# Kernel tuning notes

Measured on AMD Instinct MI355X. Metric: run time of the kernel, lower is better.

Reference implementation:

```python
import jax, jax.numpy as jnp
import numpy as np

B, S = 16, 4096
E_ENC, E_DEC, H = 1024, 1024, 512


def setup_inputs() -> dict:
    key = jax.random.key(0)
    ks = jax.random.split(key, 8)
    sc_e = 1.0 / np.sqrt(E_ENC)
    sc_d = 1.0 / np.sqrt(E_DEC)
    sc_h = 1.0 / np.sqrt(H)
    return {
        "encoder_hiddens": jax.random.normal(ks[0], (B, S, E_ENC), jnp.float32),
        "decoder_hidden": jax.random.normal(ks[1], (B, E_DEC), jnp.float32),
        "We": jax.random.uniform(ks[2], (E_ENC, H), jnp.float32, -sc_e, sc_e),
        "be": jax.random.uniform(ks[3], (H,), jnp.float32, -sc_e, sc_e),
        "Wd": jax.random.uniform(ks[4], (E_DEC, H), jnp.float32, -sc_d, sc_d),
        "bd": jax.random.uniform(ks[5], (H,), jnp.float32, -sc_d, sc_d),
        "Wo": jax.random.uniform(ks[6], (H, 1), jnp.float32, -sc_h, sc_h),
        "bo": jax.random.uniform(ks[7], (1,), jnp.float32, -sc_h, sc_h),
    }


def reference(encoder_hiddens, decoder_hidden, We, be, Wd, bd, Wo, bo):
    # Additive (Bahdanau) attention.
    # enc_proj: [B,S,H]; dec_proj: [B,1,H] broadcast over sequence.
    enc_proj = jnp.einsum("bse,eh->bsh", encoder_hiddens, We) + be
    dec_proj = jnp.einsum("bd,dh->bh", decoder_hidden, Wd) + bd
    e = jnp.tanh(enc_proj + dec_proj[:, None, :])          # [B,S,H]
    scores = jnp.einsum("bsh,h->bs", e, Wo[:, 0]) + bo[0]  # [B,S]
    attn = jax.nn.softmax(scores, axis=-1)                 # [B,S]
    context = jnp.einsum("bs,bse->be", attn, encoder_hiddens)  # [B,E_ENC]
    return context
```

## Files before the change

kernel.cpp:

```cpp
#include <hip/hip_runtime.h>
#include <hip/hip_bf16.h>
#include <math.h>

#define B_ 16
#define S_ 4096
#define E_ 1024
#define H_ 512

typedef short bf16x8 __attribute__((ext_vector_type(8)));
typedef unsigned short u16x8 __attribute__((ext_vector_type(8)));
typedef float f32x4 __attribute__((ext_vector_type(4)));

__device__ inline unsigned short f2bf(float x) {
    __hip_bfloat16 h = __float2bfloat16(x);
    return *(unsigned short*)&h;
}
__device__ inline float bf2f(unsigned short u) {
    unsigned int x = ((unsigned int)u) << 16;
    float f;
    __builtin_memcpy(&f, &x, 4);
    return f;
}

__global__ __launch_bounds__(256) void we_transpose_kernel(
    const float* __restrict__ We, unsigned short* __restrict__ WeT) {
    __shared__ float sT[64][65];
    int k0 = (blockIdx.x >> 3) * 64;
    int n0 = (blockIdx.x & 7) * 64;
    int t = threadIdx.x;
#pragma unroll
    for (int p = 0; p < 16; ++p) {
        int idx = p * 256 + t;
        int k = idx >> 6, n = idx & 63;
        sT[n][k] = We[(size_t)(k0 + k) * H_ + n0 + n];
    }
    __syncthreads();
#pragma unroll
    for (int p = 0; p < 16; ++p) {
        int idx = p * 256 + t;
        int n = idx >> 6, k = idx & 63;
        WeT[(size_t)(n0 + n) * E_ + k0 + k] = f2bf(sT[n][k]);
    }
}

__global__ __launch_bounds__(256) void dp_kernel(const float* __restrict__ dec,
                                                 const float* __restrict__ Wd,
                                                 const float* __restrict__ bd,
                                                 const float* __restrict__ be,
                                                 float* __restrict__ dp) {
    int b = blockIdx.x >> 3;
    int hc = blockIdx.x & 7;
    int t = threadIdx.x;
    int h = hc * 64 + (t & 63);
    int ec = t >> 6;
    const float* dr = dec + b * E_ + ec * 256;
    const float* wp = Wd + (size_t)(ec * 256) * H_ + h;
    float acc = 0.f;
#pragma unroll 8
    for (int e = 0; e < 256; ++e) acc = fmaf(dr[e], wp[(size_t)e * H_], acc);
    __shared__ float red[4][64];
    red[ec][t & 63] = acc;
    __syncthreads();
    if (t < 64) {
        int hh = hc * 64 + t;
        dp[b * H_ + hh] = red[0][t] + red[1][t] + red[2][t] + red[3][t] + bd[hh] + be[hh];
    }
}

#define BM 64
#define BK 32
#define LDA 40

template <int WRITE_ENCB>
__global__ __launch_bounds__(256, 2) void scores_mfma_kernel(
    const float* __restrict__ enc, const unsigned short* __restrict__ WeT,
    const float* __restrict__ Wo, const float* __restrict__ dp,
    float* __restrict__ scores, unsigned short* __restrict__ encB) {
    __shared__ unsigned short sA[BM * LDA];
    __shared__ float sRed[4][BM];

    int tid = threadIdx.x;
    int wave = tid >> 6, lane = tid & 63;
    int quad = lane >> 4, l16 = lane & 15;
    size_t m0 = (size_t)blockIdx.x * BM;
    int b = (int)(m0 >> 12);

    int srow = tid >> 3;
    int skoff = (tid & 7) * 4;
    const float* encP = enc + (m0 + srow) * E_ + skoff;
    unsigned short* encBP = encB + (m0 + srow) * E_ + skoff;
    unsigned short* sAw = sA + srow * LDA + skoff;

    f32x4 acc[4][8];
#pragma unroll
    for (int i = 0; i < 4; ++i)
#pragma unroll
        for (int j = 0; j < 8; ++j) acc[i][j] = (f32x4)0.f;

    float4 cur0 = *(const float4*)(encP);
    float4 cur1 = *(const float4*)(encP + 32 * E_);

    const unsigned short* wrow = WeT + (size_t)(wave * 128 + l16) * E_ + quad * 8;

    for (int k0 = 0; k0 < E_; k0 += BK) {
        ushort4 u0, u1;
        u0.x = f2bf(cur0.x); u0.y = f2bf(cur0.y); u0.z = f2bf(cur0.z); u0.w = f2bf(cur0.w);
        u1.x = f2bf(cur1.x); u1.y = f2bf(cur1.y); u1.z = f2bf(cur1.z); u1.w = f2bf(cur1.w);
        *(ushort4*)(sAw) = u0;
        *(ushort4*)(sAw + 32 * LDA) = u1;
        if (WRITE_ENCB) {
            *(ushort4*)(encBP + k0) = u0;
            *(ushort4*)(encBP + k0 + 32 * E_) = u1;
        }
        __syncthreads();
        if (k0 + BK < E_) {
            cur0 = *(const float4*)(encP + k0 + BK);
            cur1 = *(const float4*)(encP + k0 + BK + 32 * E_);
        }
        bf16x8 aR[4];
#pragma unroll
        for (int i = 0; i < 4; ++i)
            aR[i] = *(const bf16x8*)(sA + (i * 16 + l16) * LDA + quad * 8);
#pragma unroll
        for (int j = 0; j < 8; ++j) {
            bf16x8 bR = *(const bf16x8*)(wrow + (size_t)j * 16 * E_ + k0);
#pragma unroll
            for (int i = 0; i < 4; ++i)
                acc[i][j] = __builtin_amdgcn_mfma_f32_16x16x32_bf16(aR[i], bR, acc[i][j], 0, 0, 0);
        }
        __syncthreads();
    }

    float dpv[8], wov[8];
    const float* dpb = dp + b * H_;
#pragma unroll
    for (int j = 0; j < 8; ++j) {
        int h = wave * 128 + j * 16 + l16;
        dpv[j] = dpb[h];
        wov[j] = Wo[h];
    }
#pragma unroll
    for (int i = 0; i < 4; ++i)
#pragma unroll
        for (int r = 0; r < 4; ++r) {
            float s = 0.f;
#pragma unroll
            for (int j = 0; j < 8; ++j) {
                float x = acc[i][j][r] + dpv[j];
                float e = __expf(2.f * x);
                s += (1.f - 2.f / (e + 1.f)) * wov[j];
            }
            s += __shfl_xor(s, 1, 64);
            s += __shfl_xor(s, 2, 64);
            s += __shfl_xor(s, 4, 64);
            s += __shfl_xor(s, 8, 64);
            if (l16 == 0) sRed[wave][i * 16 + quad * 4 + r] = s;
        }
    __syncthreads();
    if (tid < BM) {
        int s_in = (int)(m0 & (S_ - 1)) + tid;
        scores[(size_t)b * S_ + s_in] =
            sRed[0][tid] + sRed[1][tid] + sRed[2][tid] + sRed[3][tid];
    }
}

__global__ __launch_bounds__(256) void softmax_kernel(float* __restrict__ sc) {
    int b = blockIdx.x;
    float* row = sc + (size_t)b * S_;
    int tid = threadIdx.x;
    float v[16];
    float m = -1e30f;
#pragma unroll
    for (int i = 0; i < 16; ++i) {
        v[i] = row[i * 256 + tid];
        m = fmaxf(m, v[i]);
    }
    for (int off = 32; off; off >>= 1) m = fmaxf(m, __shfl_xor(m, off, 64));
    __shared__ float redm[4];
    __shared__ float reds[4];
    if ((tid & 63) == 0) redm[tid >> 6] = m;
    __syncthreads();
    m = fmaxf(fmaxf(redm[0], redm[1]), fmaxf(redm[2], redm[3]));
    float s = 0.f;
#pragma unroll
    for (int i = 0; i < 16; ++i) {
        v[i] = __expf(v[i] - m);
        s += v[i];
    }
    for (int off = 32; off; off >>= 1) s += __shfl_xor(s, off, 64);
    if ((tid & 63) == 0) reds[tid >> 6] = s;
    __syncthreads();
    s = reds[0] + reds[1] + reds[2] + reds[3];
    float inv = 1.f / s;
#pragma unroll
    for (int i = 0; i < 16; ++i) row[i * 256 + tid] = v[i] * inv;
}

__global__ __launch_bounds__(256) void ctx_partial_bf16(
    const unsigned short* __restrict__ encB, const float* __restrict__ attn,
    float* __restrict__ part) {
    int b = blockIdx.x >> 5;
    int c = blockIdx.x & 31;
    int s0 = c * 128;
    int tid = threadIdx.x;
    __shared__ float w[128];
    if (tid < 128) w[tid] = attn[(size_t)b * S_ + s0 + tid];
    __syncthreads();
    int e8 = (tid & 127) * 8;
    int sh = tid >> 7;
    const unsigned short* base = encB + ((size_t)b * S_ + s0 + sh * 64) * E_ + e8;
    const float* wp = w + sh * 64;
    float acc[8];
#pragma unroll
    for (int t = 0; t < 8; ++t) acc[t] = 0.f;
    for (int s = 0; s < 64; s += 4) {
        u16x8 v0 = *(const u16x8*)(base + (size_t)(s + 0) * E_);
        u16x8 v1 = *(const u16x8*)(base + (size_t)(s + 1) * E_);
        u16x8 v2 = *(const u16x8*)(base + (size_t)(s + 2) * E_);
        u16x8 v3 = *(const u16x8*)(base + (size_t)(s + 3) * E_);
        float w0 = wp[s], w1 = wp[s + 1], w2 = wp[s + 2], w3 = wp[s + 3];
#pragma unroll
        for (int t = 0; t < 8; ++t) {
            acc[t] = fmaf(w0, bf2f(v0[t]), acc[t]);
            acc[t] = fmaf(w1, bf2f(v1[t]), acc[t]);
            acc[t] = fmaf(w2, bf2f(v2[t]), acc[t]);
            acc[t] = fmaf(w3, bf2f(v3[t]), acc[t]);
        }
    }
    float* po = part + ((size_t)(b * 64 + c * 2 + sh)) * E_ + e8;
    *(float4*)(po) = make_float4(acc[0], acc[1], acc[2], acc[3]);
    *(float4*)(po + 4) = make_float4(acc[4], acc[5], acc[6], acc[7]);
}

__global__ __launch_bounds__(256) void ctx_partial_f32(
    const float* __restrict__ enc, const float* __restrict__ attn,
    float* __restrict__ part) {
    int b = blockIdx.x >> 5;
    int c = blockIdx.x & 31;
    int s0 = c * 128;
    int tid = threadIdx.x;
    __shared__ float w[128];
    if (tid < 128) w[tid] = attn[(size_t)b * S_ + s0 + tid];
    __syncthreads();
    const float* base = enc + ((size_t)b * S_ + s0) * E_ + tid * 4;
    float4 acc = make_float4(0.f, 0.f, 0.f, 0.f);
    for (int s = 0; s < 128; s += 2) {
        float4 v0 = *(const float4*)(base + (size_t)s * E_);
        float4 v1 = *(const float4*)(base + (size_t)(s + 1) * E_);
        float w0 = w[s], w1 = w[s + 1];
        acc.x = fmaf(w0, v0.x, acc.x); acc.y = fmaf(w0, v0.y, acc.y);
        acc.z = fmaf(w0, v0.z, acc.z); acc.w = fmaf(w0, v0.w, acc.w);
        acc.x = fmaf(w1, v1.x, acc.x); acc.y = fmaf(w1, v1.y, acc.y);
        acc.z = fmaf(w1, v1.z, acc.z); acc.w = fmaf(w1, v1.w, acc.w);
    }
    *(float4*)(part + ((size_t)(b * 32 + c)) * E_ + tid * 4) = acc;
}

__global__ __launch_bounds__(256) void ctx_reduce(const float* __restrict__ part,
                                                  float* __restrict__ out, int nch) {
    int idx = blockIdx.x * 256 + threadIdx.x;
    int b = idx >> 10;
    int e = idx & 1023;
    const float* p = part + (size_t)b * nch * E_ + e;
    float s = 0.f;
    for (int c = 0; c < nch; ++c) s += p[(size_t)c * E_];
    out[idx] = s;
}

extern "C" void kernel_launch(void* const* d_in, const int* in_sizes, int n_in,
                              void* d_out, int out_size, void* d_ws, size_t ws_size,
                              hipStream_t stream) {
    const float* enc = (const float*)d_in[0];
    const float* dec = (const float*)d_in[1];
    const float* We  = (const float*)d_in[2];
    const float* be  = (const float*)d_in[3];
    const float* Wd  = (const float*)d_in[4];
    const float* bd  = (const float*)d_in[5];
    const float* Wo  = (const float*)d_in[6];
    float* out = (float*)d_out;

    char* w = (char*)d_ws;
    unsigned short* WeT = (unsigned short*)w;
    float* dp = (float*)(w + (1 << 20));
    float* scores = (float*)(w + (1 << 20) + (32 << 10));
    float* part = (float*)(w + (2 << 20));
    unsigned short* encB = (unsigned short*)(w + (8 << 20));
    const size_t need_bf16 = (size_t)(8 << 20) + (size_t)B_ * S_ * E_ * 2;
    bool use_bf16_ctx = ws_size >= need_bf16;

    we_transpose_kernel<<<128, 256, 0, stream>>>(We, WeT);
    dp_kernel<<<B_ * 8, 256, 0, stream>>>(dec, Wd, bd, be, dp);
    if (use_bf16_ctx) {
        scores_mfma_kernel<1><<<B_ * S_ / BM, 256, 0, stream>>>(enc, WeT, Wo, dp, scores, encB);
        softmax_kernel<<<B_, 256, 0, stream>>>(scores);
        ctx_partial_bf16<<<B_ * 32, 256, 0, stream>>>(encB, scores, part);
        ctx_reduce<<<B_ * E_ / 256, 256, 0, stream>>>(part, out, 64);
    } else {
        scores_mfma_kernel<0><<<B_ * S_ / BM, 256, 0, stream>>>(enc, WeT, Wo, dp, scores, encB);
        softmax_kernel<<<B_, 256, 0, stream>>>(scores);
        ctx_partial_f32<<<B_ * 32, 256, 0, stream>>>(enc, scores, part);
        ctx_reduce<<<B_ * E_ / 256, 256, 0, stream>>>(part, out, 32);
    }
}
```

Measured before the change: 572.1 us.

## Stage chunked bf16 We tiles in LDS with 128-row, 8-wave MFMA blocks

The scores GEMM kernel now uses 512-thread blocks covering 128 rows, arranged as 2x4 waves. Each K-chunk of the bf16 weight matrix is staged in shared memory from a new K-chunked layout written by a merged prep kernel, instead of every wave reading B fragments directly from global memory. This is meant to cut redundant global/L2 traffic for We and halve the number of blocks, at the cost of more LDS use per block and lower occupancy. The transpose and decoder-projection kernels are fused into one launch, and the partial-context reduction gets four independent accumulators.

```diff
diff --git a/kernel.cpp b/kernel.cpp
--- a/kernel.cpp
+++ b/kernel.cpp
@@ -22,74 +22,75 @@
     return f;
 }
 
-__global__ __launch_bounds__(256) void we_transpose_kernel(
-    const float* __restrict__ We, unsigned short* __restrict__ WeT) {
-    __shared__ float sT[64][65];
-    int k0 = (blockIdx.x >> 3) * 64;
-    int n0 = (blockIdx.x & 7) * 64;
+__global__ __launch_bounds__(256) void prep_kernel(
+    const float* __restrict__ We, const float* __restrict__ dec,
+    const float* __restrict__ Wd, const float* __restrict__ bd,
+    const float* __restrict__ be, unsigned short* __restrict__ WeTc,
+    float* __restrict__ dp) {
     int t = threadIdx.x;
-#pragma unroll
-    for (int p = 0; p < 16; ++p) {
-        int idx = p * 256 + t;
-        int k = idx >> 6, n = idx & 63;
-        sT[n][k] = We[(size_t)(k0 + k) * H_ + n0 + n];
-    }
-    __syncthreads();
-#pragma unroll
-    for (int p = 0; p < 16; ++p) {
-        int idx = p * 256 + t;
-        int n = idx >> 6, k = idx & 63;
-        WeT[(size_t)(n0 + n) * E_ + k0 + k] = f2bf(sT[n][k]);
-    }
-}
-
-__global__ __launch_bounds__(256) void dp_kernel(const float* __restrict__ dec,
-                                                 const float* __restrict__ Wd,
-                                                 const float* __restrict__ bd,
-                                                 const float* __restrict__ be,
-                                                 float* __restrict__ dp) {
-    int b = blockIdx.x >> 3;
-    int hc = blockIdx.x & 7;
-    int t = threadIdx.x;
-    int h = hc * 64 + (t & 63);
-    int ec = t >> 6;
-    const float* dr = dec + b * E_ + ec * 256;
-    const float* wp = Wd + (size_t)(ec * 256) * H_ + h;
-    float acc = 0.f;
+    if (blockIdx.x < 128) {
+        __shared__ float sT[64][65];
+        int k0 = (blockIdx.x >> 3) * 64;
+        int n0 = (blockIdx.x & 7) * 64;
+#pragma unroll
+        for (int p = 0; p < 16; ++p) {
+            int idx = p * 256 + t;
+            int k = idx >> 6, n = idx & 63;
+            sT[n][k] = We[(size_t)(k0 + k) * H_ + n0 + n];
+        }
+        __syncthreads();
+#pragma unroll
+        for (int p = 0; p < 16; ++p) {
+            int idx = p * 256 + t;
+            int n = idx >> 6, k = idx & 63;
+            int kk = k0 + k, nn = n0 + n;
+            WeTc[(size_t)(kk >> 5) * 16384 + nn * 32 + (kk & 31)] = f2bf(sT[n][k]);
+        }
+    } else {
+        int b = blockIdx.x - 128;
+        __shared__ float sdec[E_];
+#pragma unroll
+        for (int i = 0; i < 4; ++i) sdec[i * 256 + t] = dec[b * E_ + i * 256 + t];
+        __syncthreads();
+        float a0 = 0.f, a1 = 0.f;
 #pragma unroll 8
-    for (int e = 0; e < 256; ++e) acc = fmaf(dr[e], wp[(size_t)e * H_], acc);
-    __shared__ float red[4][64];
-    red[ec][t & 63] = acc;
-    __syncthreads();
-    if (t < 64) {
-        int hh = hc * 64 + t;
-        dp[b * H_ + hh] = red[0][t] + red[1][t] + red[2][t] + red[3][t] + bd[hh] + be[hh];
-    }
-}
-
-#define BM 64
+        for (int e = 0; e < E_; ++e) {
+            float d = sdec[e];
+            a0 = fmaf(d, Wd[(size_t)e * H_ + t], a0);
+            a1 = fmaf(d, Wd[(size_t)e * H_ + 256 + t], a1);
+        }
+        dp[b * H_ + t] = a0 + bd[t] + be[t];
+        dp[b * H_ + 256 + t] = a1 + bd[256 + t] + be[256 + t];
+    }
+}
+
+#define BM 128
 #define BK 32
-#define LDA 40
+#define LDW 40
+#define NCH (E_ / BK)
 
 template <int WRITE_ENCB>
-__global__ __launch_bounds__(256, 2) void scores_mfma_kernel(
-    const float* __restrict__ enc, const unsigned short* __restrict__ WeT,
+__global__ __launch_bounds__(512, 2) void scores_mfma_kernel(
+    const float* __restrict__ enc, const unsigned short* __restrict__ WeTc,
     const float* __restrict__ Wo, const float* __restrict__ dp,
     float* __restrict__ scores, unsigned short* __restrict__ encB) {
-    __shared__ unsigned short sA[BM * LDA];
+    __shared__ unsigned short sA[BM * LDW];
+    __shared__ unsigned short sB[H_ * LDW];
     __shared__ float sRed[4][BM];
 
     int tid = threadIdx.x;
     int wave = tid >> 6, lane = tid & 63;
     int quad = lane >> 4, l16 = lane & 15;
+    int wm = wave & 1, wn = wave >> 1;
     size_t m0 = (size_t)blockIdx.x * BM;
     int b = (int)(m0 >> 12);
 
-    int srow = tid >> 3;
-    int skoff = (tid & 7) * 4;
-    const float* encP = enc + (m0 + srow) * E_ + skoff;
-    unsigned short* encBP = encB + (m0 + srow) * E_ + skoff;
-    unsigned short* sAw = sA + srow * LDA + skoff;
+    int ar = tid >> 2;
+    int ac = (tid & 3) * 8;
+    const float* encP = enc + (m0 + ar) * E_ + ac;
+    unsigned short* sAw = sA + ar * LDW + ac;
+    unsigned short* encBP = encB + (m0 + ar) * E_ + ac;
+    unsigned short* sBw = sB + tid * LDW;
 
     f32x4 acc[4][8];
 #pragma unroll
@@ -97,45 +98,52 @@
 #pragma unroll
         for (int j = 0; j < 8; ++j) acc[i][j] = (f32x4)0.f;
 
-    float4 cur0 = *(const float4*)(encP);
-    float4 cur1 = *(const float4*)(encP + 32 * E_);
-
-    const unsigned short* wrow = WeT + (size_t)(wave * 128 + l16) * E_ + quad * 8;
-
-    for (int k0 = 0; k0 < E_; k0 += BK) {
-        ushort4 u0, u1;
-        u0.x = f2bf(cur0.x); u0.y = f2bf(cur0.y); u0.z = f2bf(cur0.z); u0.w = f2bf(cur0.w);
-        u1.x = f2bf(cur1.x); u1.y = f2bf(cur1.y); u1.z = f2bf(cur1.z); u1.w = f2bf(cur1.w);
-        *(ushort4*)(sAw) = u0;
-        *(ushort4*)(sAw + 32 * LDA) = u1;
-        if (WRITE_ENCB) {
-            *(ushort4*)(encBP + k0) = u0;
-            *(ushort4*)(encBP + k0 + 32 * E_) = u1;
-        }
+    float4 pa0 = *(const float4*)(encP);
+    float4 pa1 = *(const float4*)(encP + 4);
+    const u16x8* wp0 = (const u16x8*)(WeTc + (size_t)tid * 32);
+    u16x8 pb0 = wp0[0], pb1 = wp0[1], pb2 = wp0[2], pb3 = wp0[3];
+
+    const unsigned short* sAr = sA + (wm * 64 + l16) * LDW + quad * 8;
+    const unsigned short* sBr = sB + (wn * 128 + l16) * LDW + quad * 8;
+
+    for (int c = 0; c < NCH; ++c) {
+        u16x8 ua;
+        ua[0] = f2bf(pa0.x); ua[1] = f2bf(pa0.y);
+        ua[2] = f2bf(pa0.z); ua[3] = f2bf(pa0.w);
+        ua[4] = f2bf(pa1.x); ua[5] = f2bf(pa1.y);
+        ua[6] = f2bf(pa1.z); ua[7] = f2bf(pa1.w);
         __syncthreads();
-        if (k0 + BK < E_) {
-            cur0 = *(const float4*)(encP + k0 + BK);
-            cur1 = *(const float4*)(encP + k0 + BK + 32 * E_);
+        *(u16x8*)sAw = ua;
+        *(u16x8*)(sBw) = pb0;
+        *(u16x8*)(sBw + 8) = pb1;
+        *(u16x8*)(sBw + 16) = pb2;
+        *(u16x8*)(sBw + 24) = pb3;
+        if (WRITE_ENCB) *(u16x8*)(encBP + c * BK) = ua;
+        __syncthreads();
+        if (c + 1 < NCH) {
+            pa0 = *(const float4*)(encP + (c + 1) * BK);
+            pa1 = *(const float4*)(encP + (c + 1) * BK + 4);
+            const u16x8* wpn = (const u16x8*)(WeTc + (size_t)(c + 1) * 16384 + (size_t)tid * 32);
+            pb0 = wpn[0]; pb1 = wpn[1]; pb2 = wpn[2]; pb3 = wpn[3];
         }
         bf16x8 aR[4];
 #pragma unroll
         for (int i = 0; i < 4; ++i)
-            aR[i] = *(const bf16x8*)(sA + (i * 16 + l16) * LDA + quad * 8);
+            aR[i] = *(const bf16x8*)(sAr + i * 16 * LDW);
 #pragma unroll
         for (int j = 0; j < 8; ++j) {
-            bf16x8 bR = *(const bf16x8*)(wrow + (size_t)j * 16 * E_ + k0);
+            bf16x8 bR = *(const bf16x8*)(sBr + j * 16 * LDW);
 #pragma unroll
             for (int i = 0; i < 4; ++i)
                 acc[i][j] = __builtin_amdgcn_mfma_f32_16x16x32_bf16(aR[i], bR, acc[i][j], 0, 0, 0);
         }
-        __syncthreads();
     }
 
     float dpv[8], wov[8];
     const float* dpb = dp + b * H_;
 #pragma unroll
     for (int j = 0; j < 8; ++j) {
-        int h = wave * 128 + j * 16 + l16;
+        int h = wn * 128 + j * 16 + l16;
         dpv[j] = dpb[h];
         wov[j] = Wo[h];
     }
@@ -154,7 +162,7 @@
             s += __shfl_xor(s, 2, 64);
             s += __shfl_xor(s, 4, 64);
             s += __shfl_xor(s, 8, 64);
-            if (l16 == 0) sRed[wave][i * 16 + quad * 4 + r] = s;
+            if (l16 == 0) sRed[wn][wm * 64 + i * 16 + quad * 4 + r] = s;
         }
     __syncthreads();
     if (tid < BM) {
@@ -262,9 +270,14 @@
     int b = idx >> 10;
     int e = idx & 1023;
     const float* p = part + (size_t)b * nch * E_ + e;
-    float s = 0.f;
-    for (int c = 0; c < nch; ++c) s += p[(size_t)c * E_];
-    out[idx] = s;
+    float s0 = 0.f, s1 = 0.f, s2 = 0.f, s3 = 0.f;
+    for (int c = 0; c < nch; c += 4) {
+        s0 += p[(size_t)(c + 0) * E_];
+        s1 += p[(size_t)(c + 1) * E_];
+        s2 += p[(size_t)(c + 2) * E_];
+        s3 += p[(size_t)(c + 3) * E_];
+    }
+    out[idx] = (s0 + s1) + (s2 + s3);
 }
 
 extern "C" void kernel_launch(void* const* d_in, const int* in_sizes, int n_in,
@@ -280,7 +293,7 @@
     float* out = (float*)d_out;
 
     char* w = (char*)d_ws;
-    unsigned short* WeT = (unsigned short*)w;
+    unsigned short* WeTc = (unsigned short*)w;
     float* dp = (float*)(w + (1 << 20));
     float* scores = (float*)(w + (1 << 20) + (32 << 10));
     float* part = (float*)(w + (2 << 20));
@@ -288,15 +301,14 @@
     const size_t need_bf16 = (size_t)(8 << 20) + (size_t)B_ * S_ * E_ * 2;
     bool use_bf16_ctx = ws_size >= need_bf16;
 
-    we_transpose_kernel<<<128, 256, 0, stream>>>(We, WeT);
-    dp_kernel<<<B_ * 8, 256, 0, stream>>>(dec, Wd, bd, be, dp);
+    prep_kernel<<<144, 256, 0, stream>>>(We, dec, Wd, bd, be, WeTc, dp);
     if (use_bf16_ctx) {
-        scores_mfma_kernel<1><<<B_ * S_ / BM, 256, 0, stream>>>(enc, WeT, Wo, dp, scores, encB);
+        scores_mfma_kernel<1><<<B_ * S_ / BM, 512, 0, stream>>>(enc, WeTc, Wo, dp, scores, encB);
         softmax_kernel<<<B_, 256, 0, stream>>>(scores);
         ctx_partial_bf16<<<B_ * 32, 256, 0, stream>>>(encB, scores, part);
         ctx_reduce<<<B_ * E_ / 256, 256, 0, stream>>>(part, out, 64);
     } else {
-        scores_mfma_kernel<0><<<B_ * S_ / BM, 256, 0, stream>>>(enc, WeT, Wo, dp, scores, encB);
+        scores_mfma_kernel<0><<<B_ * S_ / BM, 512, 0, stream>>>(enc, WeTc, Wo, dp, scores, encB);
         softmax_kernel<<<B_, 256, 0, stream>>>(scores);
         ctx_partial_f32<<<B_ * 32, 256, 0, stream>>>(enc, scores, part);
         ctx_reduce<<<B_ * E_ / 256, 256, 0, stream>>>(part, out, 32);
```

Result: no change. 574.6 us (+0.4%).
